# Kernel tuning notes

Measured on AMD Instinct MI355X. Metric: run time of the kernel, lower is better.

The kernel has to match this reference:

```python
import jax, jax.numpy as jnp
import numpy as np

B, N, ATTR, H, OUT, STEPS = 8, 4096, 16, 64, 1, 8


def setup_inputs() -> dict:
    key = jax.random.key(0)
    ks = jax.random.split(key, 12)
    attr_matrix = jax.random.normal(ks[0], (B, N, ATTR), jnp.float32)
    adj_matrix = (jax.random.uniform(ks[1], (B, N, N)) < 0.01).astype(jnp.float32)
    s = float(1.0 / np.sqrt(H))
    u = lambda k, shape: jax.random.uniform(k, shape, jnp.float32, -s, s)
    Wi = jax.random.normal(ks[2], (H, ATTR), jnp.float32) * float(np.sqrt(2.0 / ATTR))  # kaiming
    bi = jnp.zeros((H,), jnp.float32)
    Wz = u(ks[3], (H, 3 * H)); bz = u(ks[4], (H,))
    Wr = u(ks[5], (H, 3 * H)); br = u(ks[6], (H,))
    Wh = u(ks[7], (H, 3 * H)); bh = u(ks[8], (H,))
    Wo = jax.random.normal(ks[9], (OUT, H), jnp.float32) * float(np.sqrt(2.0 / (H + OUT)))  # xavier
    bo = jnp.zeros((OUT,), jnp.float32)
    return dict(attr_matrix=attr_matrix, adj_matrix=adj_matrix, Wi=Wi, bi=bi,
                Wz=Wz, bz=bz, Wr=Wr, br=br, Wh=Wh, bh=bh, Wo=Wo, bo=bo)


def reference(attr_matrix, adj_matrix, Wi, bi, Wz, bz, Wr, br, Wh, bh, Wo, bo):
    # initial node states: (B, N, H)
    h = jax.nn.relu(attr_matrix @ Wi.T + bi)
    A_in = adj_matrix
    A_out = jnp.swapaxes(adj_matrix, -1, -2)
    for _ in range(STEPS):
        a_in = jnp.einsum('bij,bjh->bih', A_in, h)
        a_out = jnp.einsum('bij,bjh->bih', A_out, h)
        inp = jnp.concatenate([a_in, a_out], axis=-1)           # (B, N, 2H)
        xs = jnp.concatenate([inp, h], axis=-1)                  # (B, N, 3H)
        z = jax.nn.sigmoid(xs @ Wz.T + bz)
        r = jax.nn.sigmoid(xs @ Wr.T + br)
        hn = jnp.tanh(jnp.concatenate([inp, r * h], axis=-1) @ Wh.T + bh)
        h = (1.0 - z) * h + z * hn
    return h @ Wo.T + bo  # (B, N, OUT)
```

## Files before the change

### kernel.cpp

```cpp
#include <hip/hip_runtime.h>
#include <hip/hip_fp16.h>
#include <stdint.h>

#define BB 8
#define NN 4096
#define ATTRD 16
#define HD 64
#define STEPS 8
#define NODES (BB*NN)
#define ECAP 96
#define KPAD 196

typedef _Float16 half8 __attribute__((ext_vector_type(8)));
typedef float floatx4 __attribute__((ext_vector_type(4)));
typedef unsigned long long ull;

__global__ void init_h_kernel(const float* __restrict__ attr, const float* __restrict__ Wi,
                              const float* __restrict__ bi, float* __restrict__ h,
                              __half* __restrict__ h16) {
    int idx = blockIdx.x * blockDim.x + threadIdx.x;
    if (idx >= NODES * HD) return;
    int node = idx >> 6, l = idx & 63;
    const float* a = attr + node * ATTRD;
    const float* w = Wi + l * ATTRD;
    float acc = bi[l];
#pragma unroll
    for (int k = 0; k < ATTRD; k++) acc += a[k] * w[k];
    float r = acc > 0.f ? acc : 0.f;
    h[idx] = r;
    h16[idx] = __float2half(r);
}

__global__ void wprep_kernel(const float* __restrict__ Wz, const float* __restrict__ Wr,
                             const float* __restrict__ Wh,
                             _Float16* __restrict__ wf_hi, _Float16* __restrict__ wf_lo) {
    int t = blockIdx.x * blockDim.x + threadIdx.x;
    if (t >= 3 * 4 * 6 * 64 * 8) return;
    int mat = t / 12288, rem = t % 12288;
    int tile = rem / 3072, rem2 = rem % 3072;
    int kc = rem2 / 512, rem3 = rem2 % 512;
    int lane = rem3 / 8, j = rem3 % 8;
    int k = kc * 32 + (lane >> 4) * 8 + j;
    int och = tile * 16 + (lane & 15);
    const float* W = (mat == 0) ? Wz : (mat == 1) ? Wr : Wh;
    float v = W[och * 192 + k];
    _Float16 hi = (_Float16)v;
    wf_hi[t] = hi;
    wf_lo[t] = (_Float16)(v - (float)hi);
}

__global__ __launch_bounds__(256) void count_rows_kernel(const float4* __restrict__ A4,
                                                         int* __restrict__ cnt_in,
                                                         int* __restrict__ edge_in) {
    int wave = threadIdx.x >> 6, l = threadIdx.x & 63;
    int row = blockIdx.x * 4 + wave;
    const float4* rp = A4 + (size_t)row * 1024;
    ull mask_lt = (l == 63) ? ~0ull >> 1 : ((1ull << (l + 1)) - 1) >> 1;
    float4 v[16];
#pragma unroll
    for (int t = 0; t < 16; t++) v[t] = rp[t * 64 + l];
    int colbase = (row >> 12) << 12;
    int run = 0;
    int* erow = edge_in + row * ECAP;
#pragma unroll
    for (int t = 0; t < 16; t++) {
        ull b0 = __ballot(v[t].x != 0.f);
        ull b1 = __ballot(v[t].y != 0.f);
        ull b2 = __ballot(v[t].z != 0.f);
        ull b3 = __ballot(v[t].w != 0.f);
        int pre = __popcll(b0 & mask_lt) + __popcll(b1 & mask_lt) +
                  __popcll(b2 & mask_lt) + __popcll(b3 & mask_lt);
        float vv[4] = {v[t].x, v[t].y, v[t].z, v[t].w};
        int jbase = (t * 64 + l) * 4;
        int inner = 0;
#pragma unroll
        for (int q = 0; q < 4; q++) {
            if (vv[q] != 0.f) {
                int slot = run + pre + inner;
                if (slot < ECAP) erow[slot] = colbase | (jbase + q);
                inner++;
            }
        }
        run += __popcll(b0) + __popcll(b1) + __popcll(b2) + __popcll(b3);
    }
    if (l == 0) cnt_in[row] = run;
}

__global__ __launch_bounds__(256) void transpose_kernel(const int* __restrict__ cnt_in,
                                                        const int* __restrict__ edge_in,
                                                        int* __restrict__ cnt_out,
                                                        int* __restrict__ edge_out) {
    int wave = threadIdx.x >> 6, l = threadIdx.x & 63;
    int row = blockIdx.x * 4 + wave;
    int n = cnt_in[row]; if (n > ECAP) n = ECAP;
    for (int s = l; s < n; s += 64) {
        int j = edge_in[row * ECAP + s];
        int s2 = atomicAdd(&cnt_out[j], 1);
        if (s2 < ECAP) edge_out[j * ECAP + s2] = row;
    }
}

__global__ __launch_bounds__(256) void aggregate_kernel(
        const __half2* __restrict__ h2, const float* __restrict__ h,
        const int* __restrict__ cnt_in, const int* __restrict__ edge_in,
        const int* __restrict__ cnt_out, const int* __restrict__ edge_out,
        float* __restrict__ xs) {
    int bid = blockIdx.x;
    int batch = bid & 7;
    int group = bid >> 3;
    int wave = threadIdx.x >> 6;
    int pair = group * 4 + wave;
    int node = (batch << 12) + (pair >> 1);
    int dir = pair & 1;
    int l = threadIdx.x & 63;
    int half = l >> 5, sl = l & 31;
    int n = dir ? cnt_out[node] : cnt_in[node];
    if (n > ECAP) n = ECAP;
    const int* eidx = (dir ? edge_out : edge_in) + node * ECAP;
    float a0 = 0.f, a1 = 0.f;
    int s = 0;
    for (; s + 16 <= n; s += 16) {
        int i0 = eidx[s +  0 + half];
        int i1 = eidx[s +  2 + half];
        int i2 = eidx[s +  4 + half];
        int i3 = eidx[s +  6 + half];
        int i4 = eidx[s +  8 + half];
        int i5 = eidx[s + 10 + half];
        int i6 = eidx[s + 12 + half];
        int i7 = eidx[s + 14 + half];
        float2 f0 = __half22float2(h2[(i0 << 5) | sl]);
        float2 f1 = __half22float2(h2[(i1 << 5) | sl]);
        float2 f2 = __half22float2(h2[(i2 << 5) | sl]);
        float2 f3 = __half22float2(h2[(i3 << 5) | sl]);
        float2 f4 = __half22float2(h2[(i4 << 5) | sl]);
        float2 f5 = __half22float2(h2[(i5 << 5) | sl]);
        float2 f6 = __half22float2(h2[(i6 << 5) | sl]);
        float2 f7 = __half22float2(h2[(i7 << 5) | sl]);
        a0 += f0.x; a1 += f0.y;  a0 += f1.x; a1 += f1.y;
        a0 += f2.x; a1 += f2.y;  a0 += f3.x; a1 += f3.y;
        a0 += f4.x; a1 += f4.y;  a0 += f5.x; a1 += f5.y;
        a0 += f6.x; a1 += f6.y;  a0 += f7.x; a1 += f7.y;
    }
    for (; s + 8 <= n; s += 8) {
        int i0 = eidx[s + 0 + half];
        int i1 = eidx[s + 2 + half];
        int i2 = eidx[s + 4 + half];
        int i3 = eidx[s + 6 + half];
        float2 f0 = __half22float2(h2[(i0 << 5) | sl]);
        float2 f1 = __half22float2(h2[(i1 << 5) | sl]);
        float2 f2 = __half22float2(h2[(i2 << 5) | sl]);
        float2 f3 = __half22float2(h2[(i3 << 5) | sl]);
        a0 += f0.x; a1 += f0.y;  a0 += f1.x; a1 += f1.y;
        a0 += f2.x; a1 += f2.y;  a0 += f3.x; a1 += f3.y;
    }
    for (; s + 2 <= n; s += 2) {
        float2 f0 = __half22float2(h2[(eidx[s + half] << 5) | sl]);
        a0 += f0.x; a1 += f0.y;
    }
    if (s < n && half == 0) {
        float2 f0 = __half22float2(h2[(eidx[s] << 5) | sl]);
        a0 += f0.x; a1 += f0.y;
    }
    a0 += __shfl_xor(a0, 32);
    a1 += __shfl_xor(a1, 32);
    if (half == 0) {
        float2 st = {a0, a1};
        *(float2*)(xs + node * 192 + dir * 64 + sl * 2) = st;
    }
    if (dir == 0) xs[node * 192 + 128 + l] = h[(node << 6) | l];
}

__global__ __launch_bounds__(256) void gate_kernel(
        const float* __restrict__ xs_g,
        const _Float16* __restrict__ wf_hi, const _Float16* __restrict__ wf_lo,
        const float* __restrict__ bz, const float* __restrict__ br,
        const float* __restrict__ bh,
        float* __restrict__ h, __half* __restrict__ h16) {
    __shared__ float xs_t[16][KPAD];
    int bid = blockIdx.x;
    int base = ((bid & 7) << 12) | ((bid >> 3) << 4);
    int tid = threadIdx.x;
    {
        const float4* src = (const float4*)(xs_g + base * 192);
#pragma unroll
        for (int i = 0; i < 3; i++) {
            int idx = tid + i * 256;
            float4 v = src[idx];
            int nl = idx / 48, kb = (idx % 48) * 4;
            *(float4*)&xs_t[nl][kb] = v;
        }
    }
    __syncthreads();
    int wave = tid >> 6, lane = tid & 63;
    int m = lane & 15, q = lane >> 4;
    int ch = wave * 16 + m;
    const half8* WH = (const half8*)wf_hi;
    const half8* WL = (const half8*)wf_lo;

    floatx4 accz = {0.f, 0.f, 0.f, 0.f};
    floatx4 accr = {0.f, 0.f, 0.f, 0.f};
#pragma unroll
    for (int kc = 0; kc < 6; kc++) {
        const float* xr = &xs_t[m][kc * 32 + q * 8];
        float4 xa = *(const float4*)xr;
        float4 xb = *(const float4*)(xr + 4);
        float xv[8] = {xa.x, xa.y, xa.z, xa.w, xb.x, xb.y, xb.z, xb.w};
        half8 ahi, alo;
#pragma unroll
        for (int j = 0; j < 8; j++) {
            _Float16 hj = (_Float16)xv[j];
            ahi[j] = hj;
            alo[j] = (_Float16)(xv[j] - (float)hj);
        }
        half8 bzh = WH[((0 * 4 + wave) * 6 + kc) * 64 + lane];
        half8 bzl = WL[((0 * 4 + wave) * 6 + kc) * 64 + lane];
        half8 brh = WH[((1 * 4 + wave) * 6 + kc) * 64 + lane];
        half8 brl = WL[((1 * 4 + wave) * 6 + kc) * 64 + lane];
        accz = __builtin_amdgcn_mfma_f32_16x16x32_f16(ahi, bzh, accz, 0, 0, 0);
        accz = __builtin_amdgcn_mfma_f32_16x16x32_f16(alo, bzh, accz, 0, 0, 0);
        accz = __builtin_amdgcn_mfma_f32_16x16x32_f16(ahi, bzl, accz, 0, 0, 0);
        accr = __builtin_amdgcn_mfma_f32_16x16x32_f16(ahi, brh, accr, 0, 0, 0);
        accr = __builtin_amdgcn_mfma_f32_16x16x32_f16(alo, brh, accr, 0, 0, 0);
        accr = __builtin_amdgcn_mfma_f32_16x16x32_f16(ahi, brl, accr, 0, 0, 0);
    }
    float bzv = bz[ch], brv = br[ch], bhv = bh[ch];
    float zreg[4], hvreg[4], rh[4];
#pragma unroll
    for (int rg = 0; rg < 4; rg++) {
        int nl = q * 4 + rg;
        float z = 1.f / (1.f + __expf(-(accz[rg] + bzv)));
        float r = 1.f / (1.f + __expf(-(accr[rg] + brv)));
        float hv = xs_t[nl][128 + ch];
        zreg[rg] = z; hvreg[rg] = hv; rh[rg] = r * hv;
    }
    __syncthreads();
#pragma unroll
    for (int rg = 0; rg < 4; rg++) xs_t[q * 4 + rg][128 + ch] = rh[rg];
    __syncthreads();

    floatx4 acch = {0.f, 0.f, 0.f, 0.f};
#pragma unroll
    for (int kc = 0; kc < 6; kc++) {
        const float* xr = &xs_t[m][kc * 32 + q * 8];
        float4 xa = *(const float4*)xr;
        float4 xb = *(const float4*)(xr + 4);
        float xv[8] = {xa.x, xa.y, xa.z, xa.w, xb.x, xb.y, xb.z, xb.w};
        half8 ahi, alo;
#pragma unroll
        for (int j = 0; j < 8; j++) {
            _Float16 hj = (_Float16)xv[j];
            ahi[j] = hj;
            alo[j] = (_Float16)(xv[j] - (float)hj);
        }
        half8 bhh = WH[((2 * 4 + wave) * 6 + kc) * 64 + lane];
        half8 bhl = WL[((2 * 4 + wave) * 6 + kc) * 64 + lane];
        acch = __builtin_amdgcn_mfma_f32_16x16x32_f16(ahi, bhh, acch, 0, 0, 0);
        acch = __builtin_amdgcn_mfma_f32_16x16x32_f16(alo, bhh, acch, 0, 0, 0);
        acch = __builtin_amdgcn_mfma_f32_16x16x32_f16(ahi, bhl, acch, 0, 0, 0);
    }
    __syncthreads();
#pragma unroll
    for (int rg = 0; rg < 4; rg++) {
        int nl = q * 4 + rg;
        float pre = acch[rg] + bhv;
        float th = 2.f / (1.f + __expf(-2.f * pre)) - 1.f;
        float hv = hvreg[rg];
        xs_t[nl][ch] = hv + zreg[rg] * (th - hv);
    }
    __syncthreads();
    {
        int f = tid * 4;
        int nl = f >> 6, c = f & 63;
        float4 v = *(const float4*)&xs_t[nl][c];
        int gi = ((base + nl) << 6) | c;
        *(float4*)&h[gi] = v;
        __half2 p0 = {__float2half(v.x), __float2half(v.y)};
        __half2 p1 = {__float2half(v.z), __float2half(v.w)};
        *(__half2*)&h16[gi] = p0;
        *(__half2*)&h16[gi + 2] = p1;
    }
}

__global__ void out_kernel(const float* __restrict__ h, const float* __restrict__ Wo,
                           const float* __restrict__ bo, float* __restrict__ out) {
    int wid = (blockIdx.x * blockDim.x + threadIdx.x) >> 6;
    int l = threadIdx.x & 63;
    if (wid >= NODES) return;
    float p = h[(wid << 6) | l] * Wo[l];
#pragma unroll
    for (int off = 32; off > 0; off >>= 1) p += __shfl_down(p, off);
    if (l == 0) out[wid] = p + bo[0];
}

extern "C" void kernel_launch(void* const* d_in, const int* in_sizes, int n_in,
                              void* d_out, int out_size, void* d_ws, size_t ws_size,
                              hipStream_t stream) {
    const float* attr = (const float*)d_in[0];
    const float* adj  = (const float*)d_in[1];
    const float* Wi   = (const float*)d_in[2];
    const float* bi   = (const float*)d_in[3];
    const float* Wz   = (const float*)d_in[4];
    const float* bz   = (const float*)d_in[5];
    const float* Wr   = (const float*)d_in[6];
    const float* br   = (const float*)d_in[7];
    const float* Wh   = (const float*)d_in[8];
    const float* bh   = (const float*)d_in[9];
    const float* Wo   = (const float*)d_in[10];
    const float* bo   = (const float*)d_in[11];
    float* out = (float*)d_out;

    char* ws = (char*)d_ws;
    size_t off = 0;
    auto carve = [&](size_t bytes) { void* p = ws + off; off = (off + bytes + 255) & ~(size_t)255; return p; };
    float* h      = (float*)carve((size_t)NODES * HD * 4);
    __half* h16   = (__half*)carve((size_t)NODES * HD * 2);
    float* xs     = (float*)carve((size_t)NODES * 192 * 4);
    _Float16* wf_hi = (_Float16*)carve(3 * 4 * 6 * 64 * 8 * 2);
    _Float16* wf_lo = (_Float16*)carve(3 * 4 * 6 * 64 * 8 * 2);
    int* cnt_in   = (int*)carve((size_t)NODES * 4);
    int* cnt_out  = (int*)carve((size_t)NODES * 4);
    int* edge_in  = (int*)carve((size_t)NODES * ECAP * 4);
    int* edge_out = (int*)carve((size_t)NODES * ECAP * 4);

    hipMemsetAsync(cnt_out, 0, (size_t)NODES * 4, stream);

    init_h_kernel<<<NODES * HD / 256, 256, 0, stream>>>(attr, Wi, bi, h, h16);
    wprep_kernel<<<(3 * 4 * 6 * 64 * 8 + 255) / 256, 256, 0, stream>>>(Wz, Wr, Wh, wf_hi, wf_lo);
    count_rows_kernel<<<NODES / 4, 256, 0, stream>>>((const float4*)adj, cnt_in, edge_in);
    transpose_kernel<<<NODES / 4, 256, 0, stream>>>(cnt_in, edge_in, cnt_out, edge_out);

    for (int step = 0; step < STEPS; ++step) {
        aggregate_kernel<<<NODES * 2 * 64 / 256, 256, 0, stream>>>(
            (const __half2*)h16, h, cnt_in, edge_in, cnt_out, edge_out, xs);
        gate_kernel<<<NODES / 16, 256, 0, stream>>>(xs, wf_hi, wf_lo, bz, br, bh, h, h16);
    }
    out_kernel<<<NODES * HD / 256, 256, 0, stream>>>(h, Wo, bo, out);
}
```

Baseline: 1.255 ms.

## Gather neighbor rows with 16-byte loads, eight edges per wave iteration

```diff
diff --git a/kernel.cpp b/kernel.cpp
--- a/kernel.cpp
+++ b/kernel.cpp
@@ -19,7 +19,11 @@
                               const float* __restrict__ bi, float* __restrict__ h,
                               __half* __restrict__ h16) {
     int idx = blockIdx.x * blockDim.x + threadIdx.x;
-    if (idx >= NODES * HD) return;
+    if (idx >= (NODES + 1) * HD) return;
+    if (idx >= NODES * HD) {
+        h16[idx] = __float2half(0.f);
+        return;
+    }
     int node = idx >> 6, l = idx & 63;
     const float* a = attr + node * ATTRD;
     const float* w = Wi + l * ATTRD;
@@ -101,7 +105,7 @@
 }
 
 __global__ __launch_bounds__(256) void aggregate_kernel(
-        const __half2* __restrict__ h2, const float* __restrict__ h,
+        const uint4* __restrict__ h4, const float* __restrict__ h,
         const int* __restrict__ cnt_in, const int* __restrict__ edge_in,
         const int* __restrict__ cnt_out, const int* __restrict__ edge_out,
         float* __restrict__ xs) {
@@ -113,59 +117,39 @@
     int node = (batch << 12) + (pair >> 1);
     int dir = pair & 1;
     int l = threadIdx.x & 63;
-    int half = l >> 5, sl = l & 31;
+    int sub = l >> 3;
+    int part = l & 7;
     int n = dir ? cnt_out[node] : cnt_in[node];
     if (n > ECAP) n = ECAP;
-    const int* eidx = (dir ? edge_out : edge_in) + node * ECAP;
-    float a0 = 0.f, a1 = 0.f;
-    int s = 0;
-    for (; s + 16 <= n; s += 16) {
-        int i0 = eidx[s +  0 + half];
-        int i1 = eidx[s +  2 + half];
-        int i2 = eidx[s +  4 + half];
-        int i3 = eidx[s +  6 + half];
-        int i4 = eidx[s +  8 + half];
-        int i5 = eidx[s + 10 + half];
-        int i6 = eidx[s + 12 + half];
-        int i7 = eidx[s + 14 + half];
-        float2 f0 = __half22float2(h2[(i0 << 5) | sl]);
-        float2 f1 = __half22float2(h2[(i1 << 5) | sl]);
-        float2 f2 = __half22float2(h2[(i2 << 5) | sl]);
-        float2 f3 = __half22float2(h2[(i3 << 5) | sl]);
-        float2 f4 = __half22float2(h2[(i4 << 5) | sl]);
-        float2 f5 = __half22float2(h2[(i5 << 5) | sl]);
-        float2 f6 = __half22float2(h2[(i6 << 5) | sl]);
-        float2 f7 = __half22float2(h2[(i7 << 5) | sl]);
-        a0 += f0.x; a1 += f0.y;  a0 += f1.x; a1 += f1.y;
-        a0 += f2.x; a1 += f2.y;  a0 += f3.x; a1 += f3.y;
-        a0 += f4.x; a1 += f4.y;  a0 += f5.x; a1 += f5.y;
-        a0 += f6.x; a1 += f6.y;  a0 += f7.x; a1 += f7.y;
-    }
-    for (; s + 8 <= n; s += 8) {
-        int i0 = eidx[s + 0 + half];
-        int i1 = eidx[s + 2 + half];
-        int i2 = eidx[s + 4 + half];
-        int i3 = eidx[s + 6 + half];
-        float2 f0 = __half22float2(h2[(i0 << 5) | sl]);
-        float2 f1 = __half22float2(h2[(i1 << 5) | sl]);
-        float2 f2 = __half22float2(h2[(i2 << 5) | sl]);
-        float2 f3 = __half22float2(h2[(i3 << 5) | sl]);
-        a0 += f0.x; a1 += f0.y;  a0 += f1.x; a1 += f1.y;
-        a0 += f2.x; a1 += f2.y;  a0 += f3.x; a1 += f3.y;
-    }
-    for (; s + 2 <= n; s += 2) {
-        float2 f0 = __half22float2(h2[(eidx[s + half] << 5) | sl]);
-        a0 += f0.x; a1 += f0.y;
-    }
-    if (s < n && half == 0) {
-        float2 f0 = __half22float2(h2[(eidx[s] << 5) | sl]);
-        a0 += f0.x; a1 += f0.y;
-    }
-    a0 += __shfl_xor(a0, 32);
-    a1 += __shfl_xor(a1, 32);
-    if (half == 0) {
-        float2 st = {a0, a1};
-        *(float2*)(xs + node * 192 + dir * 64 + sl * 2) = st;
+    const int* erow = (dir ? edge_out : edge_in) + node * ECAP;
+    int e0 = erow[l];
+    int e1 = erow[64 + (l & 31)];
+    float a0 = 0.f, a1 = 0.f, a2 = 0.f, a3 = 0.f, a4 = 0.f, a5 = 0.f, a6 = 0.f, a7 = 0.f;
+    for (int s = 0; s < n; s += 8) {
+        int il = s + sub;
+        int gidx = (il < 64) ? __shfl(e0, il) : __shfl(e1, il - 64);
+        gidx = (il < n) ? gidx : NODES;
+        uint4 g = h4[(gidx << 3) | part];
+        float2 p0 = __half22float2(*(__half2*)&g.x);
+        float2 p1 = __half22float2(*(__half2*)&g.y);
+        float2 p2 = __half22float2(*(__half2*)&g.z);
+        float2 p3 = __half22float2(*(__half2*)&g.w);
+        a0 += p0.x; a1 += p0.y; a2 += p1.x; a3 += p1.y;
+        a4 += p2.x; a5 += p2.y; a6 += p3.x; a7 += p3.y;
+    }
+#pragma unroll
+    for (int off = 8; off < 64; off <<= 1) {
+        a0 += __shfl_xor(a0, off); a1 += __shfl_xor(a1, off);
+        a2 += __shfl_xor(a2, off); a3 += __shfl_xor(a3, off);
+        a4 += __shfl_xor(a4, off); a5 += __shfl_xor(a5, off);
+        a6 += __shfl_xor(a6, off); a7 += __shfl_xor(a7, off);
+    }
+    if (l < 8) {
+        float4 s0 = {a0, a1, a2, a3};
+        float4 s1 = {a4, a5, a6, a7};
+        float* dst = xs + node * 192 + dir * 64 + l * 8;
+        *(float4*)dst = s0;
+        *(float4*)(dst + 4) = s1;
     }
     if (dir == 0) xs[node * 192 + 128 + l] = h[(node << 6) | l];
 }
@@ -313,7 +297,7 @@
     size_t off = 0;
     auto carve = [&](size_t bytes) { void* p = ws + off; off = (off + bytes + 255) & ~(size_t)255; return p; };
     float* h      = (float*)carve((size_t)NODES * HD * 4);
-    __half* h16   = (__half*)carve((size_t)NODES * HD * 2);
+    __half* h16   = (__half*)carve((size_t)(NODES + 1) * HD * 2);
     float* xs     = (float*)carve((size_t)NODES * 192 * 4);
     _Float16* wf_hi = (_Float16*)carve(3 * 4 * 6 * 64 * 8 * 2);
     _Float16* wf_lo = (_Float16*)carve(3 * 4 * 6 * 64 * 8 * 2);
@@ -324,14 +308,14 @@
 
     hipMemsetAsync(cnt_out, 0, (size_t)NODES * 4, stream);
 
-    init_h_kernel<<<NODES * HD / 256, 256, 0, stream>>>(attr, Wi, bi, h, h16);
+    init_h_kernel<<<((NODES + 1) * HD + 255) / 256, 256, 0, stream>>>(attr, Wi, bi, h, h16);
     wprep_kernel<<<(3 * 4 * 6 * 64 * 8 + 255) / 256, 256, 0, stream>>>(Wz, Wr, Wh, wf_hi, wf_lo);
     count_rows_kernel<<<NODES / 4, 256, 0, stream>>>((const float4*)adj, cnt_in, edge_in);
     transpose_kernel<<<NODES / 4, 256, 0, stream>>>(cnt_in, edge_in, cnt_out, edge_out);
 
     for (int step = 0; step < STEPS; ++step) {
         aggregate_kernel<<<NODES * 2 * 64 / 256, 256, 0, stream>>>(
-            (const __half2*)h16, h, cnt_in, edge_in, cnt_out, edge_out, xs);
+            (const uint4*)h16, h, cnt_in, edge_in, cnt_out, edge_out, xs);
         gate_kernel<<<NODES / 16, 256, 0, stream>>>(xs, wf_hi, wf_lo, bz, br, bh, h, h16);
     }
     out_kernel<<<NODES * HD / 256, 256, 0, stream>>>(h, Wo, bo, out);
```

Result: faster. 1.225 ms (-2.4%).
